# Kernel tuning notes

Hardware: AMD Instinct MI355X
Metric: run time of the kernel (lower is better)

## Reference

```python
import jax, jax.numpy as jnp
import numpy as np

GRID = 10
C_IN = 4          # input_dim // (grid*grid) = 400 // 100
HID = 128         # lstm hidden_dim
NV = 6            # num_vehicles
PH = 10           # pred_horizon
BN_EPS = 1e-5


def setup_inputs() -> dict:
    key = jax.random.key(0)
    ks = jax.random.split(key, 20)
    def n(k, shape, scale=0.05):
        return jax.random.normal(k, shape, jnp.float32) * scale
    return {
        "observations": jax.random.normal(ks[0], (1024, 32, 400), jnp.float32),
        # CNN
        "conv1_w": n(ks[1], (16, C_IN, 3, 3)), "conv1_b": n(ks[2], (16,)),
        "conv2_w": n(ks[3], (32, 16, 3, 3)), "conv2_b": n(ks[4], (32,)),
        # FCN (BatchNorm in eval mode: running stats + affine)
        "fc1_w": n(ks[5], (128, 128)), "fc1_b": n(ks[6], (128,)),
        "bn1_gamma": jnp.ones((128,), jnp.float32), "bn1_beta": jnp.zeros((128,), jnp.float32),
        "bn1_mean": jnp.zeros((128,), jnp.float32), "bn1_var": jnp.ones((128,), jnp.float32),
        "fc2_w": n(ks[7], (64, 128)), "fc2_b": n(ks[8], (64,)),
        "bn2_gamma": jnp.ones((64,), jnp.float32), "bn2_beta": jnp.zeros((64,), jnp.float32),
        "bn2_mean": jnp.zeros((64,), jnp.float32), "bn2_var": jnp.ones((64,), jnp.float32),
        # encoder LSTM (torch gate order i,f,g,o; b = b_ih + b_hh fused)
        "enc_w_ih": n(ks[9], (4 * HID, 64)), "enc_w_hh": n(ks[10], (4 * HID, HID)),
        "enc_b": n(ks[11], (4 * HID,)),
        # decoder LSTM
        "dec_w_ih": n(ks[12], (4 * HID, HID)), "dec_w_hh": n(ks[13], (4 * HID, HID)),
        "dec_b": n(ks[14], (4 * HID,)),
        # output head
        "out_w": n(ks[15], (2 * NV, HID)), "out_b": n(ks[16], (2 * NV,)),
    }


def _conv(x, w, b):
    y = jax.lax.conv_general_dilated(x, w, (1, 1), "SAME",
                                     dimension_numbers=("NCHW", "OIHW", "NCHW"))
    return y + b[None, :, None, None]


def _maxpool2(x):
    # MaxPool2d(2,2) with floor (drops odd trailing row/col) == VALID
    return jax.lax.reduce_window(x, -jnp.inf, jax.lax.max, (1, 1, 2, 2), (1, 1, 2, 2), "VALID")


def _bn(x, g, b, m, v):
    return (x - m) * jax.lax.rsqrt(v + BN_EPS) * g + b


def _lstm_cell(x, h, c, w_ih, w_hh, b):
    gates = x @ w_ih.T + h @ w_hh.T + b
    i, f, g, o = jnp.split(gates, 4, axis=-1)
    c_new = jax.nn.sigmoid(f) * c + jax.nn.sigmoid(i) * jnp.tanh(g)
    h_new = jax.nn.sigmoid(o) * jnp.tanh(c_new)
    return h_new, c_new


def reference(observations, conv1_w, conv1_b, conv2_w, conv2_b,
              fc1_w, fc1_b, bn1_gamma, bn1_beta, bn1_mean, bn1_var,
              fc2_w, fc2_b, bn2_gamma, bn2_beta, bn2_mean, bn2_var,
              enc_w_ih, enc_w_hh, enc_b, dec_w_ih, dec_w_hh, dec_b,
              out_w, out_b):
    B, T, D = observations.shape
    # ---- fuse the per-frame Python loop: batch all B*T frames at once ----
    x = observations.reshape(B * T, C_IN, GRID, GRID)
    x = _maxpool2(jax.nn.relu(_conv(x, conv1_w, conv1_b)))   # [BT,16,5,5]
    x = _maxpool2(jax.nn.relu(_conv(x, conv2_w, conv2_b)))   # [BT,32,2,2]
    x = x.reshape(B * T, -1)                                 # [BT,128]
    x = jax.nn.relu(_bn(x @ fc1_w.T + fc1_b, bn1_gamma, bn1_beta, bn1_mean, bn1_var))
    x = jax.nn.relu(_bn(x @ fc2_w.T + fc2_b, bn2_gamma, bn2_beta, bn2_mean, bn2_var))
    feats = x.reshape(B, T, 64)

    # ---- encoder LSTM ----
    h0 = jnp.zeros((B, HID), feats.dtype)
    c0 = jnp.zeros((B, HID), feats.dtype)
    def enc_step(carry, xt):
        h, c = carry
        h, c = _lstm_cell(xt, h, c, enc_w_ih, enc_w_hh, enc_b)
        return (h, c), h
    (h_n, c_n), hs = jax.lax.scan(enc_step, (h0, c0), jnp.swapaxes(feats, 0, 1))
    dec_x = hs[-1]  # encoder_output[:, -1]

    def dec_step(carry, _):
        x_in, h, c = carry
        h, c = _lstm_cell(x_in, h, c, dec_w_ih, dec_w_hh, dec_b)
        pred = h @ out_w.T + out_b
        return (h, h, c), pred
    _, preds = jax.lax.scan(dec_step, (dec_x, h_n, c_n), None, length=PH)
    return jnp.swapaxes(preds, 0, 1)  # [B, PH, 2*NV]
```

## Files before the change

kernel.cpp:

```cpp
#include <hip/hip_runtime.h>
#include <hip/hip_bf16.h>
#include <hip/hip_fp16.h>

constexpr int GT = 32768;
constexpr int TSEQ = 32;

typedef _Float16 h2 __attribute__((ext_vector_type(2)));

#if defined(__has_builtin)
#if __has_builtin(__builtin_amdgcn_fdot2)
#define FDOT2(a, b, c) __builtin_amdgcn_fdot2((a), (b), (c), false)
#endif
#endif
#ifndef FDOT2
#define FDOT2(a, b, c) fmaf((float)(a).x, (float)(b).x, fmaf((float)(a).y, (float)(b).y, (c)))
#endif

__device__ __forceinline__ h2 pack2(float a, float b) {
  h2 v; v.x = (_Float16)a; v.y = (_Float16)b; return v;
}

constexpr size_t OBS_T  = 0;
constexpr size_t POOL1H = 13107200;
constexpr size_t FEATSH = 19660800;
constexpr size_t GX     = 0;
constexpr size_t WB     = 26214400;
constexpr size_t W_C1   = WB + 0;
constexpr size_t W_C2H  = WB + 576;
constexpr size_t W_F1H  = WB + 2880;
constexpr size_t B_F1   = WB + 11072;
constexpr size_t W_F2H  = WB + 11200;
constexpr size_t B_F2   = WB + 15296;
constexpr size_t W_ENCXH= WB + 15360;
constexpr size_t W_ENCHH= WB + 31744;
constexpr size_t B_ENC  = WB + 64512;
constexpr size_t W_DECH = WB + 65024;
constexpr size_t B_DEC  = WB + 97792;

__device__ __forceinline__ float sigf(float x)  { return 1.f / (1.f + __expf(-x)); }
__device__ __forceinline__ float tanhfast(float x) { return 1.f - 2.f / (__expf(2.f * x) + 1.f); }

__global__ __launch_bounds__(256) void k_setup(
    const float* __restrict__ c1w, const float* __restrict__ c2w,
    const float* __restrict__ f1w, const float* __restrict__ f1b,
    const float* __restrict__ g1, const float* __restrict__ be1,
    const float* __restrict__ m1, const float* __restrict__ v1,
    const float* __restrict__ f2w, const float* __restrict__ f2b,
    const float* __restrict__ g2, const float* __restrict__ be2,
    const float* __restrict__ m2, const float* __restrict__ v2,
    const float* __restrict__ ewih, const float* __restrict__ ewhh, const float* __restrict__ eb,
    const float* __restrict__ dwih, const float* __restrict__ dwhh, const float* __restrict__ db,
    float* __restrict__ ws) {
  h2* wsh = (h2*)ws;
  long i = (long)blockIdx.x * 256 + threadIdx.x;
  if (i < 576)  { int c = i & 15, r = i >> 4; ws[W_C1 + i] = c1w[c * 36 + r]; return; }
  i -= 576;
  if (i < 2304) { int co = i & 31, q = i >> 5; int ci2 = q / 9, t9 = q % 9;
    wsh[W_C2H + i] = pack2(c2w[co * 144 + (2 * ci2) * 9 + t9],
                           c2w[co * 144 + (2 * ci2 + 1) * 9 + t9]); return; }
  i -= 2304;
  if (i < 8192) { int j = i & 127, q = i >> 7; int co2 = q >> 2, pos = q & 3;
    float s = g1[j] * rsqrtf(v1[j] + 1e-5f);
    wsh[W_F1H + i] = pack2(f1w[j * 128 + 8 * co2 + pos] * s,
                           f1w[j * 128 + 8 * co2 + 4 + pos] * s); return; }
  i -= 8192;
  if (i < 128) { int j = i; float s = g1[j] * rsqrtf(v1[j] + 1e-5f);
    ws[B_F1 + i] = (f1b[j] - m1[j]) * s + be1[j]; return; }
  i -= 128;
  if (i < 4096) { int j = i & 63, k2 = i >> 6;
    float s = g2[j] * rsqrtf(v2[j] + 1e-5f);
    wsh[W_F2H + i] = pack2(f2w[j * 128 + 2 * k2] * s,
                           f2w[j * 128 + 2 * k2 + 1] * s); return; }
  i -= 4096;
  if (i < 64) { int j = i; float s = g2[j] * rsqrtf(v2[j] + 1e-5f);
    ws[B_F2 + i] = (f2b[j] - m2[j]) * s + be2[j]; return; }
  i -= 64;
  if (i < 16384) { int r = i & 511, k2 = i >> 9;
    int u = r >> 2, gt = r & 3, jr = gt * 128 + u;
    wsh[W_ENCXH + i] = pack2(ewih[jr * 64 + 2 * k2], ewih[jr * 64 + 2 * k2 + 1]); return; }
  i -= 16384;
  if (i < 32768) { int r = i & 511, k2 = i >> 9;
    int u = r >> 2, gt = r & 3, jr = gt * 128 + u;
    wsh[W_ENCHH + i] = pack2(ewhh[jr * 128 + 2 * k2], ewhh[jr * 128 + 2 * k2 + 1]); return; }
  i -= 32768;
  if (i < 512) { int u = i >> 2, gt = i & 3; ws[B_ENC + i] = eb[gt * 128 + u]; return; }
  i -= 512;
  if (i < 32768) { int r = i & 511, k2 = i >> 9;
    int u = r >> 2, gt = r & 3, jr = gt * 128 + u;
    wsh[W_DECH + i] = pack2(dwih[jr * 128 + 2 * k2] + dwhh[jr * 128 + 2 * k2],
                            dwih[jr * 128 + 2 * k2 + 1] + dwhh[jr * 128 + 2 * k2 + 1]); return; }
  i -= 32768;
  if (i < 512) { int u = i >> 2, gt = i & 3; ws[B_DEC + i] = db[gt * 128 + u]; return; }
}

__global__ __launch_bounds__(256) void k_transpose(const float* __restrict__ obs,
                                                   float* __restrict__ obsT) {
  __shared__ float tile[64][65];
  int tp0 = blockIdx.x * 64;
  int b0  = blockIdx.y * 64;
  int q     = threadIdx.x & 15;
  int rbase = threadIdx.x >> 4;
  #pragma unroll
  for (int rr = 0; rr < 4; ++rr) {
    int row = rbase + rr * 16;
    const float4 v = *(const float4*)(obs + (size_t)(b0 + row) * 12800 + tp0 + q * 4);
    tile[row][q * 4 + 0] = v.x;
    tile[row][q * 4 + 1] = v.y;
    tile[row][q * 4 + 2] = v.z;
    tile[row][q * 4 + 3] = v.w;
  }
  __syncthreads();
  int lane = threadIdx.x & 63;
  int grp  = threadIdx.x >> 6;
  for (int cc = 0; cc < 16; ++cc) {
    int col = grp * 16 + cc;
    int tp = tp0 + col;
    int t = tp / 400, p = tp % 400;
    obsT[(size_t)p * GT + t * 1024 + b0 + lane] = tile[lane][col];
  }
}

__global__ __launch_bounds__(256) void k_conv1(const float* __restrict__ obsT,
                                               const float* __restrict__ wT,
                                               const float* __restrict__ bias,
                                               h2* __restrict__ pool1h) {
  int g = blockIdx.x * 256 + threadIdx.x;
  int pos = blockIdx.y;
  int py = pos / 5, px = pos % 5;
  float acc[4][16];
  #pragma unroll
  for (int s = 0; s < 4; ++s)
    #pragma unroll
    for (int c = 0; c < 16; ++c) acc[s][c] = 0.f;

  #pragma unroll 1
  for (int ci = 0; ci < 4; ++ci) {
    float p[16];
    #pragma unroll
    for (int r = 0; r < 4; ++r) {
      int iy = 2 * py + r - 1;
      #pragma unroll
      for (int cx = 0; cx < 4; ++cx) {
        int ix = 2 * px + cx - 1;
        bool ok = ((unsigned)iy < 10u) && ((unsigned)ix < 10u);
        p[r * 4 + cx] = ok ? obsT[(size_t)(ci * 100 + iy * 10 + ix) * GT + g] : 0.f;
      }
    }
    #pragma unroll
    for (int t9 = 0; t9 < 9; ++t9) {
      int ky = t9 / 3, kx = t9 % 3;
      const float* w = wT + ((ci * 9 + t9) << 4);
      float wv[16];
      #pragma unroll
      for (int c = 0; c < 16; ++c) wv[c] = w[c];
      #pragma unroll
      for (int dy = 0; dy < 2; ++dy)
        #pragma unroll
        for (int dx = 0; dx < 2; ++dx) {
          float xv = p[(dy + ky) * 4 + (dx + kx)];
          #pragma unroll
          for (int c = 0; c < 16; ++c)
            acc[dy * 2 + dx][c] = fmaf(wv[c], xv, acc[dy * 2 + dx][c]);
        }
    }
  }
  float m[16];
  #pragma unroll
  for (int c = 0; c < 16; ++c) {
    float v = fmaxf(fmaxf(acc[0][c], acc[1][c]), fmaxf(acc[2][c], acc[3][c]));
    m[c] = fmaxf(v + bias[c], 0.f);
  }
  #pragma unroll
  for (int c2 = 0; c2 < 8; ++c2)
    pool1h[(size_t)(c2 * 25 + pos) * GT + g] = pack2(m[2 * c2], m[2 * c2 + 1]);
}

__global__ __launch_bounds__(256, 4) void k_cfx(
    const h2* __restrict__ pool1h,
    const h2* __restrict__ wc2, const float* __restrict__ c2b,
    const h2* __restrict__ wf1, const float* __restrict__ bf1,
    const h2* __restrict__ wf2, const float* __restrict__ bf2,
    h2* __restrict__ featsh) {
  const int tid = threadIdx.x;
  const int fr  = tid & 31;
  const int sl  = tid >> 5;
  const int g   = blockIdx.x * 32 + fr;
  const int pos = sl & 3;
  const int ho  = sl >> 2;

  __shared__ h2 xbuf[32 * 65];
  __shared__ h2 y1buf[32 * 65];

  const int py = pos >> 1, px = pos & 1;
  const h2 hz = pack2(0.f, 0.f);
  float acc[4][16];
  #pragma unroll
  for (int s = 0; s < 4; ++s)
    #pragma unroll
    for (int c = 0; c < 16; ++c) acc[s][c] = 0.f;

  #pragma unroll 1
  for (int ci2 = 0; ci2 < 8; ++ci2) {
    h2 p[16];
    #pragma unroll
    for (int r = 0; r < 4; ++r) {
      int iy = 2 * py + r - 1;
      #pragma unroll
      for (int cx = 0; cx < 4; ++cx) {
        int ix = 2 * px + cx - 1;
        bool ok = ((unsigned)iy < 5u) && ((unsigned)ix < 5u);
        p[r * 4 + cx] = ok ? pool1h[(size_t)(ci2 * 25 + iy * 5 + ix) * GT + g] : hz;
      }
    }
    #pragma unroll
    for (int t9 = 0; t9 < 9; ++t9) {
      int ky = t9 / 3, kx = t9 % 3;
      const h2* w = wc2 + (ci2 * 9 + t9) * 32 + ho * 16;
      h2 wv[16];
      #pragma unroll
      for (int u = 0; u < 4; ++u) *(uint4*)&wv[u * 4] = *(const uint4*)&w[u * 4];
      #pragma unroll
      for (int dy = 0; dy < 2; ++dy)
        #pragma unroll
        for (int dx = 0; dx < 2; ++dx) {
          h2 xv = p[(dy + ky) * 4 + (dx + kx)];
          #pragma unroll
          for (int c = 0; c < 16; ++c)
            acc[dy * 2 + dx][c] = FDOT2(xv, wv[c], acc[dy * 2 + dx][c]);
        }
    }
  }
  #pragma unroll
  for (int c2 = 0; c2 < 8; ++c2) {
    float va = fmaxf(fmaxf(acc[0][2 * c2], acc[1][2 * c2]),
                     fmaxf(acc[2][2 * c2], acc[3][2 * c2]));
    float vb = fmaxf(fmaxf(acc[0][2 * c2 + 1], acc[1][2 * c2 + 1]),
                     fmaxf(acc[2][2 * c2 + 1], acc[3][2 * c2 + 1]));
    float a = fmaxf(va + c2b[ho * 16 + 2 * c2], 0.f);
    float b = fmaxf(vb + c2b[ho * 16 + 2 * c2 + 1], 0.f);
    int q = (ho * 8 + c2) * 4 + pos;
    xbuf[fr * 65 + q] = pack2(a, b);
  }
  __syncthreads();

  {
    float acc1[16];
    #pragma unroll
    for (int c = 0; c < 16; ++c) acc1[c] = 0.f;
    #pragma unroll 2
    for (int q = 0; q < 64; ++q) {
      h2 xv = xbuf[fr * 65 + q];
      const h2* w = wf1 + q * 128 + sl * 16;
      h2 wv[16];
      #pragma unroll
      for (int u = 0; u < 4; ++u) *(uint4*)&wv[u * 4] = *(const uint4*)&w[u * 4];
      #pragma unroll
      for (int c = 0; c < 16; ++c) acc1[c] = FDOT2(xv, wv[c], acc1[c]);
    }
    const int j0 = sl * 16;
    #pragma unroll
    for (int c2 = 0; c2 < 8; ++c2) {
      float a = fmaxf(acc1[2 * c2] + bf1[j0 + 2 * c2], 0.f);
      float b = fmaxf(acc1[2 * c2 + 1] + bf1[j0 + 2 * c2 + 1], 0.f);
      y1buf[fr * 65 + sl * 8 + c2] = pack2(a, b);
    }
  }
  __syncthreads();

  {
    float acc2[8];
    #pragma unroll
    for (int c = 0; c < 8; ++c) acc2[c] = 0.f;
    #pragma unroll 2
    for (int k2 = 0; k2 < 64; ++k2) {
      h2 xv = y1buf[fr * 65 + k2];
      const h2* w = wf2 + k2 * 64 + sl * 8;
      h2 wv[8];
      #pragma unroll
      for (int u = 0; u < 2; ++u) *(uint4*)&wv[u * 4] = *(const uint4*)&w[u * 4];
      #pragma unroll
      for (int c = 0; c < 8; ++c) acc2[c] = FDOT2(xv, wv[c], acc2[c]);
    }
    const int j0 = sl * 8;
    #pragma unroll
    for (int c2 = 0; c2 < 4; ++c2) {
      float a = fmaxf(acc2[2 * c2] + bf2[j0 + 2 * c2], 0.f);
      float b = fmaxf(acc2[2 * c2 + 1] + bf2[j0 + 2 * c2 + 1], 0.f);
      featsh[(size_t)(sl * 4 + c2) * GT + g] = pack2(a, b);
    }
  }
}

__global__ __launch_bounds__(256, 2) void k_xgatesh(const h2* __restrict__ featsh,
                                                    const h2* __restrict__ wxh,
                                                    const float* __restrict__ br,
                                                    float* __restrict__ gx) {
  __shared__ float lbuf[256 * 68];
  int t  = blockIdx.x >> 2;
  int bq = blockIdx.x & 3;
  int b  = bq * 256 + threadIdx.x;
  int r0 = blockIdx.y * 64;
  float acc[64];
  #pragma unroll
  for (int i = 0; i < 64; ++i) acc[i] = br[r0 + i];
  const h2* xcol = featsh + (size_t)t * 1024 + b;
  #pragma unroll 1
  for (int k2 = 0; k2 < 32; ++k2) {
    h2 xv = xcol[(size_t)k2 * GT];
    const h2* w = wxh + k2 * 512 + r0;
    h2 wv[64];
    #pragma unroll
    for (int u = 0; u < 16; ++u) *(uint4*)&wv[u * 4] = *(const uint4*)&w[u * 4];
    #pragma unroll
    for (int i = 0; i < 64; ++i) acc[i] = FDOT2(xv, wv[i], acc[i]);
  }
  float* lp = lbuf + threadIdx.x * 68;
  #pragma unroll
  for (int u = 0; u < 16; ++u) {
    float4 v = make_float4(acc[4 * u], acc[4 * u + 1], acc[4 * u + 2], acc[4 * u + 3]);
    *(float4*)&lp[u * 4] = v;
  }
  __syncthreads();
  const int r4 = threadIdx.x & 15;
  const int bb = threadIdx.x >> 4;
  const size_t base = (size_t)t * 524288 + (size_t)(bq * 256) * 512 + r0;
  #pragma unroll
  for (int j = 0; j < 16; ++j) {
    int bl = j * 16 + bb;
    float4 v = *(const float4*)&lbuf[bl * 68 + r4 * 4];
    *(float4*)&gx[base + (size_t)bl * 512 + r4 * 4] = v;
  }
}

__global__ __launch_bounds__(512, 2) void k_seq8(
    const float* __restrict__ gx,
    const h2* __restrict__ WENCH, const h2* __restrict__ WDECH,
    const float* __restrict__ bdec,
    const float* __restrict__ ow, const float* __restrict__ ob,
    float* __restrict__ out) {
  const int tid = threadIdx.x;
  const int bl2 = tid & 1;
  const int kg  = (tid >> 1) & 1;
  const int g   = tid >> 2;
  const int b0  = blockIdx.x * 4 + bl2 * 2;

  __shared__ h2 hbufh[2][4 * 68];
  __shared__ h2 owl2[12 * 68];

  for (int i = tid; i < 2 * 4 * 68; i += 512) ((h2*)hbufh)[i] = pack2(0.f, 0.f);
  for (int i = tid; i < 768; i += 512) {
    int o = i >> 6, k2 = i & 63;
    owl2[o * 68 + k2] = pack2(ow[o * 128 + 2 * k2], ow[o * 128 + 2 * k2 + 1]);
  }
  const float obv = (tid < 48) ? ob[tid >> 2] : 0.f;

  h2 wreg[32][4];
  #pragma unroll
  for (int p = 0; p < 32; ++p)
    *(uint4*)wreg[p] = *(const uint4*)(WENCH + (size_t)(kg * 32 + p) * 512 + g * 4);

  float c0 = 0.f, c1 = 0.f;
  __syncthreads();
  int cur = 0;

  for (int t = 0; t < TSEQ; ++t) {
    const float4 ga = *(const float4*)(gx + (size_t)t * 524288 + (size_t)b0 * 512 + g * 4);
    const float4 gb = *(const float4*)(gx + (size_t)t * 524288 + (size_t)(b0 + 1) * 512 + g * 4);

    float acc[8];
    #pragma unroll
    for (int r = 0; r < 8; ++r) acc[r] = 0.f;

    #pragma unroll
    for (int b = 0; b < 2; ++b) {
      const h2* hp = &hbufh[cur][(bl2 * 2 + b) * 68 + kg * 32];
      #pragma unroll
      for (int pc = 0; pc < 8; ++pc) {
        h2 hh[4];
        *(uint4*)hh = *(const uint4*)&hp[pc * 4];
        #pragma unroll
        for (int j = 0; j < 4; ++j) {
          const int p = pc * 4 + j;
          acc[b * 4 + 0] = FDOT2(hh[j], wreg[p][0], acc[b * 4 + 0]);
          acc[b * 4 + 1] = FDOT2(hh[j], wreg[p][1], acc[b * 4 + 1]);
          acc[b * 4 + 2] = FDOT2(hh[j], wreg[p][2], acc[b * 4 + 2]);
          acc[b * 4 + 3] = FDOT2(hh[j], wreg[p][3], acc[b * 4 + 3]);
        }
      }
    }
    float D[8];
    #pragma unroll
    for (int r = 0; r < 8; ++r) D[r] = acc[r] + __shfl_xor(acc[r], 2, 64);

    const float gi0 = D[0] + ga.x, gf0 = D[1] + ga.y, gg0 = D[2] + ga.z, go0 = D[3] + ga.w;
    const float gi1 = D[4] + gb.x, gf1 = D[5] + gb.y, gg1 = D[6] + gb.z, go1 = D[7] + gb.w;
    c0 = sigf(gf0) * c0 + sigf(gi0) * tanhfast(gg0);
    c1 = sigf(gf1) * c1 + sigf(gi1) * tanhfast(gg1);
    const float hn0 = sigf(go0) * tanhfast(c0);
    const float hn1 = sigf(go1) * tanhfast(c1);
    if (kg == 0) {
      _Float16* hf = (_Float16*)&hbufh[cur ^ 1][0];
      hf[(bl2 * 2 + 0) * 136 + g] = (_Float16)hn0;
      hf[(bl2 * 2 + 1) * 136 + g] = (_Float16)hn1;
    }
    __syncthreads();
    cur ^= 1;
  }

  #pragma unroll
  for (int p = 0; p < 32; ++p)
    *(uint4*)wreg[p] = *(const uint4*)(WDECH + (size_t)(kg * 32 + p) * 512 + g * 4);
  const float4 bd = *(const float4*)(bdec + g * 4);

  for (int t = 0; t < 10; ++t) {
    float acc[8];
    #pragma unroll
    for (int r = 0; r < 8; ++r) acc[r] = 0.f;

    #pragma unroll
    for (int b = 0; b < 2; ++b) {
      const h2* hp = &hbufh[cur][(bl2 * 2 + b) * 68 + kg * 32];
      #pragma unroll
      for (int pc = 0; pc < 8; ++pc) {
        h2 hh[4];
        *(uint4*)hh = *(const uint4*)&hp[pc * 4];
        #pragma unroll
        for (int j = 0; j < 4; ++j) {
          const int p = pc * 4 + j;
          acc[b * 4 + 0] = FDOT2(hh[j], wreg[p][0], acc[b * 4 + 0]);
          acc[b * 4 + 1] = FDOT2(hh[j], wreg[p][1], acc[b * 4 + 1]);
          acc[b * 4 + 2] = FDOT2(hh[j], wreg[p][2], acc[b * 4 + 2]);
          acc[b * 4 + 3] = FDOT2(hh[j], wreg[p][3], acc[b * 4 + 3]);
        }
      }
    }
    float D[8];
    #pragma unroll
    for (int r = 0; r < 8; ++r) D[r] = acc[r] + __shfl_xor(acc[r], 2, 64);

    const float gi0 = D[0] + bd.x, gf0 = D[1] + bd.y, gg0 = D[2] + bd.z, go0 = D[3] + bd.w;
    const float gi1 = D[4] + bd.x, gf1 = D[5] + bd.y, gg1 = D[6] + bd.z, go1 = D[7] + bd.w;
    c0 = sigf(gf0) * c0 + sigf(gi0) * tanhfast(gg0);
    c1 = sigf(gf1) * c1 + sigf(gi1) * tanhfast(gg1);
    const float hn0 = sigf(go0) * tanhfast(c0);
    const float hn1 = sigf(go1) * tanhfast(c1);
    if (kg == 0) {
      _Float16* hf = (_Float16*)&hbufh[cur ^ 1][0];
      hf[(bl2 * 2 + 0) * 136 + g] = (_Float16)hn0;
      hf[(bl2 * 2 + 1) * 136 + g] = (_Float16)hn1;
    }
    __syncthreads();
    cur ^= 1;
    if (tid < 48) {
      const int o  = tid >> 2;
      const int bh = tid & 3;
      const h2* hh = &hbufh[cur][bh * 68];
      const h2* wo = &owl2[o * 68];
      float oacc = obv;
      #pragma unroll
      for (int k2 = 0; k2 < 64; ++k2) oacc = FDOT2(hh[k2], wo[k2], oacc);
      out[(blockIdx.x * 4 + bh) * 120 + t * 12 + o] = oacc;
    }
  }
}

extern "C" void kernel_launch(void* const* d_in, const int* in_sizes, int n_in,
                              void* d_out, int out_size, void* d_ws, size_t ws_size,
                              hipStream_t stream) {
  const float* obs  = (const float*)d_in[0];
  const float* c1w  = (const float*)d_in[1];
  const float* c1b  = (const float*)d_in[2];
  const float* c2w  = (const float*)d_in[3];
  const float* c2b  = (const float*)d_in[4];
  const float* f1w  = (const float*)d_in[5];
  const float* f1b  = (const float*)d_in[6];
  const float* g1   = (const float*)d_in[7];
  const float* be1  = (const float*)d_in[8];
  const float* m1   = (const float*)d_in[9];
  const float* v1   = (const float*)d_in[10];
  const float* f2w  = (const float*)d_in[11];
  const float* f2b  = (const float*)d_in[12];
  const float* g2   = (const float*)d_in[13];
  const float* be2  = (const float*)d_in[14];
  const float* m2   = (const float*)d_in[15];
  const float* v2   = (const float*)d_in[16];
  const float* ewih = (const float*)d_in[17];
  const float* ewhh = (const float*)d_in[18];
  const float* eb   = (const float*)d_in[19];
  const float* dwih = (const float*)d_in[20];
  const float* dwhh = (const float*)d_in[21];
  const float* db   = (const float*)d_in[22];
  const float* ow   = (const float*)d_in[23];
  const float* ob   = (const float*)d_in[24];
  float* ws  = (float*)d_ws;
  h2*    wsh = (h2*)d_ws;
  float* out = (float*)d_out;

  k_setup<<<384, 256, 0, stream>>>(c1w, c2w, f1w, f1b, g1, be1, m1, v1,
                                   f2w, f2b, g2, be2, m2, v2,
                                   ewih, ewhh, eb, dwih, dwhh, db, ws);
  k_transpose<<<dim3(200, 16), 256, 0, stream>>>(obs, ws + OBS_T);
  k_conv1<<<dim3(128, 25), 256, 0, stream>>>(ws + OBS_T, ws + W_C1, c1b, wsh + POOL1H);
  k_cfx<<<1024, 256, 0, stream>>>(wsh + POOL1H, wsh + W_C2H, c2b,
                                  wsh + W_F1H, ws + B_F1,
                                  wsh + W_F2H, ws + B_F2, wsh + FEATSH);
  k_xgatesh<<<dim3(128, 8), 256, 0, stream>>>(wsh + FEATSH, wsh + W_ENCXH, ws + B_ENC,
                                              ws + GX);
  k_seq8<<<256, 512, 0, stream>>>(ws + GX, wsh + W_ENCHH, wsh + W_DECH,
                                  ws + B_DEC, ow, ob, out);
}
```

Baseline: 387.2 us.

## Split recurrent LSTM kernel to one batch row per block with finer gate split

The sequential LSTM kernel now assigns one batch element per 512-thread block (1024 blocks) instead of four, and each thread holds half as many recurrent weights, computing two gate columns. Partial sums are combined with two cross-lane shuffles and selects that rebuild the i,f,g,o gates. The intent is more parallelism and lower register pressure (launch bounds raised to allow four blocks per CU), which should shorten the per-step dependency chain. The cost is that recurrent weights are reloaded by four times as many blocks and there are more block-level syncs in total.

```diff
diff --git a/kernel.cpp b/kernel.cpp
--- a/kernel.cpp
+++ b/kernel.cpp
@@ -332,76 +332,68 @@
   }
 }
 
-__global__ __launch_bounds__(512, 2) void k_seq8(
+__global__ __launch_bounds__(512, 4) void k_seq(
     const float* __restrict__ gx,
     const h2* __restrict__ WENCH, const h2* __restrict__ WDECH,
     const float* __restrict__ bdec,
     const float* __restrict__ ow, const float* __restrict__ ob,
     float* __restrict__ out) {
   const int tid = threadIdx.x;
-  const int bl2 = tid & 1;
-  const int kg  = (tid >> 1) & 1;
+  const int kg  = tid & 1;
+  const int rp  = (tid >> 1) & 1;
   const int g   = tid >> 2;
-  const int b0  = blockIdx.x * 4 + bl2 * 2;
-
-  __shared__ h2 hbufh[2][4 * 68];
+  const int b   = blockIdx.x;
+
+  __shared__ h2 hbufh[2][68];
   __shared__ h2 owl2[12 * 68];
 
-  for (int i = tid; i < 2 * 4 * 68; i += 512) ((h2*)hbufh)[i] = pack2(0.f, 0.f);
+  for (int i = tid; i < 2 * 68; i += 512) ((h2*)hbufh)[i] = pack2(0.f, 0.f);
   for (int i = tid; i < 768; i += 512) {
     int o = i >> 6, k2 = i & 63;
     owl2[o * 68 + k2] = pack2(ow[o * 128 + 2 * k2], ow[o * 128 + 2 * k2 + 1]);
   }
-  const float obv = (tid < 48) ? ob[tid >> 2] : 0.f;
-
-  h2 wreg[32][4];
+  const float obv = (tid < 12) ? ob[tid] : 0.f;
+
+  h2 wreg[32][2];
   #pragma unroll
   for (int p = 0; p < 32; ++p)
-    *(uint4*)wreg[p] = *(const uint4*)(WENCH + (size_t)(kg * 32 + p) * 512 + g * 4);
-
-  float c0 = 0.f, c1 = 0.f;
+    *(uint2*)wreg[p] = *(const uint2*)(WENCH + (size_t)(kg * 32 + p) * 512 + g * 4 + rp * 2);
+
+  float c0 = 0.f;
   __syncthreads();
   int cur = 0;
 
   for (int t = 0; t < TSEQ; ++t) {
-    const float4 ga = *(const float4*)(gx + (size_t)t * 524288 + (size_t)b0 * 512 + g * 4);
-    const float4 gb = *(const float4*)(gx + (size_t)t * 524288 + (size_t)(b0 + 1) * 512 + g * 4);
-
-    float acc[8];
-    #pragma unroll
-    for (int r = 0; r < 8; ++r) acc[r] = 0.f;
-
-    #pragma unroll
-    for (int b = 0; b < 2; ++b) {
-      const h2* hp = &hbufh[cur][(bl2 * 2 + b) * 68 + kg * 32];
-      #pragma unroll
-      for (int pc = 0; pc < 8; ++pc) {
-        h2 hh[4];
-        *(uint4*)hh = *(const uint4*)&hp[pc * 4];
-        #pragma unroll
-        for (int j = 0; j < 4; ++j) {
-          const int p = pc * 4 + j;
-          acc[b * 4 + 0] = FDOT2(hh[j], wreg[p][0], acc[b * 4 + 0]);
-          acc[b * 4 + 1] = FDOT2(hh[j], wreg[p][1], acc[b * 4 + 1]);
-          acc[b * 4 + 2] = FDOT2(hh[j], wreg[p][2], acc[b * 4 + 2]);
-          acc[b * 4 + 3] = FDOT2(hh[j], wreg[p][3], acc[b * 4 + 3]);
-        }
+    const float4 ga = *(const float4*)(gx + (size_t)t * 524288 + (size_t)b * 512 + g * 4);
+
+    float a0 = 0.f, a1 = 0.f;
+    const h2* hp = &hbufh[cur][kg * 32];
+    #pragma unroll
+    for (int pc = 0; pc < 8; ++pc) {
+      h2 hh[4];
+      *(uint4*)hh = *(const uint4*)&hp[pc * 4];
+      #pragma unroll
+      for (int j = 0; j < 4; ++j) {
+        const int p = pc * 4 + j;
+        a0 = FDOT2(hh[j], wreg[p][0], a0);
+        a1 = FDOT2(hh[j], wreg[p][1], a1);
       }
     }
-    float D[8];
-    #pragma unroll
-    for (int r = 0; r < 8; ++r) D[r] = acc[r] + __shfl_xor(acc[r], 2, 64);
-
-    const float gi0 = D[0] + ga.x, gf0 = D[1] + ga.y, gg0 = D[2] + ga.z, go0 = D[3] + ga.w;
-    const float gi1 = D[4] + gb.x, gf1 = D[5] + gb.y, gg1 = D[6] + gb.z, go1 = D[7] + gb.w;
-    c0 = sigf(gf0) * c0 + sigf(gi0) * tanhfast(gg0);
-    c1 = sigf(gf1) * c1 + sigf(gi1) * tanhfast(gg1);
-    const float hn0 = sigf(go0) * tanhfast(c0);
-    const float hn1 = sigf(go1) * tanhfast(c1);
-    if (kg == 0) {
+    const float D0 = a0 + __shfl_xor(a0, 1, 64);
+    const float D1 = a1 + __shfl_xor(a1, 1, 64);
+    const float e0 = __shfl_xor(D0, 2, 64);
+    const float e1 = __shfl_xor(D1, 2, 64);
+    const float Di = rp ? e0 : D0;
+    const float Df = rp ? e1 : D1;
+    const float Dg = rp ? D0 : e0;
+    const float Do = rp ? D1 : e1;
+
+    const float gi = Di + ga.x, gf = Df + ga.y, gg = Dg + ga.z, go = Do + ga.w;
+    c0 = sigf(gf) * c0 + sigf(gi) * tanhfast(gg);
+    const float hn = sigf(go) * tanhfast(c0);
+    if ((tid & 3) == 0) {
       _Float16* hf = (_Float16*)&hbufh[cur ^ 1][0];
-      hf[(bl2 * 2 + 0) * 136 + g] = (_Float16)hn0;
-      hf[(bl2 * 2 + 1) * 136 + g] = (_Float16)hn1;
+      hf[g] = (_Float16)hn;
     }
     __syncthreads();
     cur ^= 1;
@@ -409,57 +401,48 @@
 
   #pragma unroll
   for (int p = 0; p < 32; ++p)
-    *(uint4*)wreg[p] = *(const uint4*)(WDECH + (size_t)(kg * 32 + p) * 512 + g * 4);
+    *(uint2*)wreg[p] = *(const uint2*)(WDECH + (size_t)(kg * 32 + p) * 512 + g * 4 + rp * 2);
   const float4 bd = *(const float4*)(bdec + g * 4);
 
   for (int t = 0; t < 10; ++t) {
-    float acc[8];
-    #pragma unroll
-    for (int r = 0; r < 8; ++r) acc[r] = 0.f;
-
-    #pragma unroll
-    for (int b = 0; b < 2; ++b) {
-      const h2* hp = &hbufh[cur][(bl2 * 2 + b) * 68 + kg * 32];
-      #pragma unroll
-      for (int pc = 0; pc < 8; ++pc) {
-        h2 hh[4];
-        *(uint4*)hh = *(const uint4*)&hp[pc * 4];
-        #pragma unroll
-        for (int j = 0; j < 4; ++j) {
-          const int p = pc * 4 + j;
-          acc[b * 4 + 0] = FDOT2(hh[j], wreg[p][0], acc[b * 4 + 0]);
-          acc[b * 4 + 1] = FDOT2(hh[j], wreg[p][1], acc[b * 4 + 1]);
-          acc[b * 4 + 2] = FDOT2(hh[j], wreg[p][2], acc[b * 4 + 2]);
-          acc[b * 4 + 3] = FDOT2(hh[j], wreg[p][3], acc[b * 4 + 3]);
-        }
+    float a0 = 0.f, a1 = 0.f;
+    const h2* hp = &hbufh[cur][kg * 32];
+    #pragma unroll
+    for (int pc = 0; pc < 8; ++pc) {
+      h2 hh[4];
+      *(uint4*)hh = *(const uint4*)&hp[pc * 4];
+      #pragma unroll
+      for (int j = 0; j < 4; ++j) {
+        const int p = pc * 4 + j;
+        a0 = FDOT2(hh[j], wreg[p][0], a0);
+        a1 = FDOT2(hh[j], wreg[p][1], a1);
       }
     }
-    float D[8];
-    #pragma unroll
-    for (int r = 0; r < 8; ++r) D[r] = acc[r] + __shfl_xor(acc[r], 2, 64);
-
-    const float gi0 = D[0] + bd.x, gf0 = D[1] + bd.y, gg0 = D[2] + bd.z, go0 = D[3] + bd.w;
-    const float gi1 = D[4] + bd.x, gf1 = D[5] + bd.y, gg1 = D[6] + bd.z, go1 = D[7] + bd.w;
-    c0 = sigf(gf0) * c0 + sigf(gi0) * tanhfast(gg0);
-    c1 = sigf(gf1) * c1 + sigf(gi1) * tanhfast(gg1);
-    const float hn0 = sigf(go0) * tanhfast(c0);
-    const float hn1 = sigf(go1) * tanhfast(c1);
-    if (kg == 0) {
+    const float D0 = a0 + __shfl_xor(a0, 1, 64);
+    const float D1 = a1 + __shfl_xor(a1, 1, 64);
+    const float e0 = __shfl_xor(D0, 2, 64);
+    const float e1 = __shfl_xor(D1, 2, 64);
+    const float Di = rp ? e0 : D0;
+    const float Df = rp ? e1 : D1;
+    const float Dg = rp ? D0 : e0;
+    const float Do = rp ? D1 : e1;
+
+    const float gi = Di + bd.x, gf = Df + bd.y, gg = Dg + bd.z, go = Do + bd.w;
+    c0 = sigf(gf) * c0 + sigf(gi) * tanhfast(gg);
+    const float hn = sigf(go) * tanhfast(c0);
+    if ((tid & 3) == 0) {
       _Float16* hf = (_Float16*)&hbufh[cur ^ 1][0];
-      hf[(bl2 * 2 + 0) * 136 + g] = (_Float16)hn0;
-      hf[(bl2 * 2 + 1) * 136 + g] = (_Float16)hn1;
+      hf[g] = (_Float16)hn;
     }
     __syncthreads();
     cur ^= 1;
-    if (tid < 48) {
-      const int o  = tid >> 2;
-      const int bh = tid & 3;
-      const h2* hh = &hbufh[cur][bh * 68];
-      const h2* wo = &owl2[o * 68];
+    if (tid < 12) {
+      const h2* hh = &hbufh[cur][0];
+      const h2* wo = &owl2[tid * 68];
       float oacc = obv;
       #pragma unroll
       for (int k2 = 0; k2 < 64; ++k2) oacc = FDOT2(hh[k2], wo[k2], oacc);
-      out[(blockIdx.x * 4 + bh) * 120 + t * 12 + o] = oacc;
+      out[b * 120 + t * 12 + tid] = oacc;
     }
   }
 }
@@ -506,6 +489,6 @@
                                   wsh + W_F2H, ws + B_F2, wsh + FEATSH);
   k_xgatesh<<<dim3(128, 8), 256, 0, stream>>>(wsh + FEATSH, wsh + W_ENCXH, ws + B_ENC,
                                               ws + GX);
-  k_seq8<<<256, 512, 0, stream>>>(ws + GX, wsh + W_ENCHH, wsh + W_DECH,
+  k_seq<<<1024, 512, 0, stream>>>(ws + GX, wsh + W_ENCHH, wsh + W_DECH,
                                   ws + B_DEC, ow, ob, out);
 }
```

Result: slower. 448.2 us (+15.8%).

## Fuse encoder input-gate projection into the LSTM sequence kernel via LDS

Applied to the files above, without the earlier changes.

The separate kernel that computed the encoder input projections (x·W_ih + b) for all timesteps and wrote a large fp32 gate tensor to global memory is removed. The sequence kernel now loads each block's feature slice into LDS and computes the input gates for 16 timesteps at a time into a roughly 132 KB LDS buffer, then runs the recurrence reading gates from LDS. This removes the global write and read of the 64 MB gate tensor and one kernel launch. In exchange the serial per-block kernel does more compute, and the large LDS footprint likely limits occupancy to one block per CU.

```diff
diff --git a/kernel.cpp b/kernel.cpp
--- a/kernel.cpp
+++ b/kernel.cpp
@@ -23,7 +23,6 @@
 constexpr size_t OBS_T  = 0;
 constexpr size_t POOL1H = 13107200;
 constexpr size_t FEATSH = 19660800;
-constexpr size_t GX     = 0;
 constexpr size_t WB     = 26214400;
 constexpr size_t W_C1   = WB + 0;
 constexpr size_t W_C2H  = WB + 576;
@@ -291,49 +290,9 @@
   }
 }
 
-__global__ __launch_bounds__(256, 2) void k_xgatesh(const h2* __restrict__ featsh,
-                                                    const h2* __restrict__ wxh,
-                                                    const float* __restrict__ br,
-                                                    float* __restrict__ gx) {
-  __shared__ float lbuf[256 * 68];
-  int t  = blockIdx.x >> 2;
-  int bq = blockIdx.x & 3;
-  int b  = bq * 256 + threadIdx.x;
-  int r0 = blockIdx.y * 64;
-  float acc[64];
-  #pragma unroll
-  for (int i = 0; i < 64; ++i) acc[i] = br[r0 + i];
-  const h2* xcol = featsh + (size_t)t * 1024 + b;
-  #pragma unroll 1
-  for (int k2 = 0; k2 < 32; ++k2) {
-    h2 xv = xcol[(size_t)k2 * GT];
-    const h2* w = wxh + k2 * 512 + r0;
-    h2 wv[64];
-    #pragma unroll
-    for (int u = 0; u < 16; ++u) *(uint4*)&wv[u * 4] = *(const uint4*)&w[u * 4];
-    #pragma unroll
-    for (int i = 0; i < 64; ++i) acc[i] = FDOT2(xv, wv[i], acc[i]);
-  }
-  float* lp = lbuf + threadIdx.x * 68;
-  #pragma unroll
-  for (int u = 0; u < 16; ++u) {
-    float4 v = make_float4(acc[4 * u], acc[4 * u + 1], acc[4 * u + 2], acc[4 * u + 3]);
-    *(float4*)&lp[u * 4] = v;
-  }
-  __syncthreads();
-  const int r4 = threadIdx.x & 15;
-  const int bb = threadIdx.x >> 4;
-  const size_t base = (size_t)t * 524288 + (size_t)(bq * 256) * 512 + r0;
-  #pragma unroll
-  for (int j = 0; j < 16; ++j) {
-    int bl = j * 16 + bb;
-    float4 v = *(const float4*)&lbuf[bl * 68 + r4 * 4];
-    *(float4*)&gx[base + (size_t)bl * 512 + r4 * 4] = v;
-  }
-}
-
-__global__ __launch_bounds__(512, 2) void k_seq8(
-    const float* __restrict__ gx,
+__global__ __launch_bounds__(512, 2) void k_seqf(
+    const h2* __restrict__ featsh,
+    const h2* __restrict__ WXH, const float* __restrict__ br,
     const h2* __restrict__ WENCH, const h2* __restrict__ WDECH,
     const float* __restrict__ bdec,
     const float* __restrict__ ow, const float* __restrict__ ob,
@@ -342,10 +301,14 @@
   const int bl2 = tid & 1;
   const int kg  = (tid >> 1) & 1;
   const int g   = tid >> 2;
-  const int b0  = blockIdx.x * 4 + bl2 * 2;
-
-  __shared__ h2 hbufh[2][4 * 68];
-  __shared__ h2 owl2[12 * 68];
+  const int bx  = tid & 3;
+  const int rw  = tid >> 2;
+  const int gb0 = blockIdx.x * 4;
+
+  __shared__ float gxl[16 * 2064];
+  __shared__ h2    featl[32 * 144];
+  __shared__ h2    hbufh[2][4 * 68];
+  __shared__ h2    owl2[12 * 68];
 
   for (int i = tid; i < 2 * 4 * 68; i += 512) ((h2*)hbufh)[i] = pack2(0.f, 0.f);
   for (int i = tid; i < 768; i += 512) {
@@ -354,57 +317,102 @@
   }
   const float obv = (tid < 48) ? ob[tid >> 2] : 0.f;
 
+  for (int i = tid; i < 4096; i += 512) {
+    int j2 = i & 31, bxs = (i >> 5) & 3, t = i >> 7;
+    featl[t * 144 + bxs * 36 + j2] = featsh[(size_t)j2 * GT + t * 1024 + gb0 + bxs];
+  }
+
+  float c0 = 0.f, c1 = 0.f;
+  int cur = 0;
   h2 wreg[32][4];
-  #pragma unroll
-  for (int p = 0; p < 32; ++p)
-    *(uint4*)wreg[p] = *(const uint4*)(WENCH + (size_t)(kg * 32 + p) * 512 + g * 4);
-
-  float c0 = 0.f, c1 = 0.f;
-  __syncthreads();
-  int cur = 0;
-
-  for (int t = 0; t < TSEQ; ++t) {
-    const float4 ga = *(const float4*)(gx + (size_t)t * 524288 + (size_t)b0 * 512 + g * 4);
-    const float4 gb = *(const float4*)(gx + (size_t)t * 524288 + (size_t)(b0 + 1) * 512 + g * 4);
-
-    float acc[8];
-    #pragma unroll
-    for (int r = 0; r < 8; ++r) acc[r] = 0.f;
-
-    #pragma unroll
-    for (int b = 0; b < 2; ++b) {
-      const h2* hp = &hbufh[cur][(bl2 * 2 + b) * 68 + kg * 32];
-      #pragma unroll
-      for (int pc = 0; pc < 8; ++pc) {
-        h2 hh[4];
-        *(uint4*)hh = *(const uint4*)&hp[pc * 4];
+
+  #pragma unroll 1
+  for (int half = 0; half < 2; ++half) {
+    __syncthreads();
+
+    const float4 bias4 = *(const float4*)(br + rw * 4);
+    #pragma unroll 1
+    for (int t8 = 0; t8 < 2; ++t8) {
+      float acc[8][4];
+      #pragma unroll
+      for (int tt = 0; tt < 8; ++tt) {
+        acc[tt][0] = bias4.x; acc[tt][1] = bias4.y;
+        acc[tt][2] = bias4.z; acc[tt][3] = bias4.w;
+      }
+      #pragma unroll 1
+      for (int k2q = 0; k2q < 8; ++k2q) {
+        h2 wv[4][4];
         #pragma unroll
-        for (int j = 0; j < 4; ++j) {
-          const int p = pc * 4 + j;
-          acc[b * 4 + 0] = FDOT2(hh[j], wreg[p][0], acc[b * 4 + 0]);
-          acc[b * 4 + 1] = FDOT2(hh[j], wreg[p][1], acc[b * 4 + 1]);
-          acc[b * 4 + 2] = FDOT2(hh[j], wreg[p][2], acc[b * 4 + 2]);
-          acc[b * 4 + 3] = FDOT2(hh[j], wreg[p][3], acc[b * 4 + 3]);
+        for (int q = 0; q < 4; ++q)
+          *(uint4*)wv[q] = *(const uint4*)(WXH + (size_t)(k2q * 4 + q) * 512 + rw * 4);
+        #pragma unroll
+        for (int tt = 0; tt < 8; ++tt) {
+          const int t = half * 16 + t8 * 8 + tt;
+          h2 xq[4];
+          *(uint4*)xq = *(const uint4*)&featl[t * 144 + bx * 36 + k2q * 4];
+          #pragma unroll
+          for (int q = 0; q < 4; ++q) {
+            acc[tt][0] = FDOT2(xq[q], wv[q][0], acc[tt][0]);
+            acc[tt][1] = FDOT2(xq[q], wv[q][1], acc[tt][1]);
+            acc[tt][2] = FDOT2(xq[q], wv[q][2], acc[tt][2]);
+            acc[tt][3] = FDOT2(xq[q], wv[q][3], acc[tt][3]);
+          }
         }
       }
-    }
-    float D[8];
-    #pragma unroll
-    for (int r = 0; r < 8; ++r) D[r] = acc[r] + __shfl_xor(acc[r], 2, 64);
-
-    const float gi0 = D[0] + ga.x, gf0 = D[1] + ga.y, gg0 = D[2] + ga.z, go0 = D[3] + ga.w;
-    const float gi1 = D[4] + gb.x, gf1 = D[5] + gb.y, gg1 = D[6] + gb.z, go1 = D[7] + gb.w;
-    c0 = sigf(gf0) * c0 + sigf(gi0) * tanhfast(gg0);
-    c1 = sigf(gf1) * c1 + sigf(gi1) * tanhfast(gg1);
-    const float hn0 = sigf(go0) * tanhfast(c0);
-    const float hn1 = sigf(go1) * tanhfast(c1);
-    if (kg == 0) {
-      _Float16* hf = (_Float16*)&hbufh[cur ^ 1][0];
-      hf[(bl2 * 2 + 0) * 136 + g] = (_Float16)hn0;
-      hf[(bl2 * 2 + 1) * 136 + g] = (_Float16)hn1;
-    }
+      #pragma unroll
+      for (int tt = 0; tt < 8; ++tt)
+        *(float4*)&gxl[(t8 * 8 + tt) * 2064 + bx * 516 + rw * 4] =
+            make_float4(acc[tt][0], acc[tt][1], acc[tt][2], acc[tt][3]);
+    }
+
+    #pragma unroll
+    for (int p = 0; p < 32; ++p)
+      *(uint4*)wreg[p] = *(const uint4*)(WENCH + (size_t)(kg * 32 + p) * 512 + g * 4);
     __syncthreads();
-    cur ^= 1;
+
+    for (int tl = 0; tl < 16; ++tl) {
+      const float4 ga = *(const float4*)&gxl[tl * 2064 + (bl2 * 2 + 0) * 516 + g * 4];
+      const float4 gb = *(const float4*)&gxl[tl * 2064 + (bl2 * 2 + 1) * 516 + g * 4];
+
+      float acc[8];
+      #pragma unroll
+      for (int r = 0; r < 8; ++r) acc[r] = 0.f;
+
+      #pragma unroll
+      for (int b = 0; b < 2; ++b) {
+        const h2* hp = &hbufh[cur][(bl2 * 2 + b) * 68 + kg * 32];
+        #pragma unroll
+        for (int pc = 0; pc < 8; ++pc) {
+          h2 hh[4];
+          *(uint4*)hh = *(const uint4*)&hp[pc * 4];
+          #pragma unroll
+          for (int j = 0; j < 4; ++j) {
+            const int p = pc * 4 + j;
+            acc[b * 4 + 0] = FDOT2(hh[j], wreg[p][0], acc[b * 4 + 0]);
+            acc[b * 4 + 1] = FDOT2(hh[j], wreg[p][1], acc[b * 4 + 1]);
+            acc[b * 4 + 2] = FDOT2(hh[j], wreg[p][2], acc[b * 4 + 2]);
+            acc[b * 4 + 3] = FDOT2(hh[j], wreg[p][3], acc[b * 4 + 3]);
+          }
+        }
+      }
+      float D[8];
+      #pragma unroll
+      for (int r = 0; r < 8; ++r) D[r] = acc[r] + __shfl_xor(acc[r], 2, 64);
+
+      const float gi0 = D[0] + ga.x, gf0 = D[1] + ga.y, gg0 = D[2] + ga.z, go0 = D[3] + ga.w;
+      const float gi1 = D[4] + gb.x, gf1 = D[5] + gb.y, gg1 = D[6] + gb.z, go1 = D[7] + gb.w;
+      c0 = sigf(gf0) * c0 + sigf(gi0) * tanhfast(gg0);
+      c1 = sigf(gf1) * c1 + sigf(gi1) * tanhfast(gg1);
+      const float hn0 = sigf(go0) * tanhfast(c0);
+      const float hn1 = sigf(go1) * tanhfast(c1);
+      if (kg == 0) {
+        _Float16* hf = (_Float16*)&hbufh[cur ^ 1][0];
+        hf[(bl2 * 2 + 0) * 136 + g] = (_Float16)hn0;
+        hf[(bl2 * 2 + 1) * 136 + g] = (_Float16)hn1;
+      }
+      __syncthreads();
+      cur ^= 1;
+    }
   }
 
   #pragma unroll
@@ -504,8 +512,7 @@
   k_cfx<<<1024, 256, 0, stream>>>(wsh + POOL1H, wsh + W_C2H, c2b,
                                   wsh + W_F1H, ws + B_F1,
                                   wsh + W_F2H, ws + B_F2, wsh + FEATSH);
-  k_xgatesh<<<dim3(128, 8), 256, 0, stream>>>(wsh + FEATSH, wsh + W_ENCXH, ws + B_ENC,
-                                              ws + GX);
-  k_seq8<<<256, 512, 0, stream>>>(ws + GX, wsh + W_ENCHH, wsh + W_DECH,
+  k_seqf<<<256, 512, 0, stream>>>(wsh + FEATSH, wsh + W_ENCXH, ws + B_ENC,
+                                  wsh + W_ENCHH, wsh + W_DECH,
                                   ws + B_DEC, ow, ob, out);
 }
```

Result: no change. 386.5 us (-0.2%).
